# Kernel tuning notes

Measured on AMD Instinct MI355X. Metric: run time of the kernel, lower is better.

Reference implementation:

```python
import jax, jax.numpy as jnp
import numpy as np

N_VN = 8000
N_CN = 4000
DV = 3
DC = 6
BATCH = 1250
CODERATE = 0.5
NUM_ITER = 5
LLR_MAX = 20.0
EPS = 1e-12


def _build_graph():
    # regular (3,6) Tanner graph: 3 layers, each layer gives every VN one edge
    # and every CN two edges (n = 2m).
    rng = np.random.RandomState(0)
    vn = np.tile(np.arange(N_VN, dtype=np.int32), DV)
    cn_layers = []
    for _ in range(DV):
        cn_layers.append(rng.permutation(np.repeat(np.arange(N_CN, dtype=np.int32), 2)))
    cn = np.concatenate(cn_layers)
    return vn, cn


def setup_inputs() -> dict:
    key = jax.random.key(0)
    k1, = jax.random.split(key, 1)
    vn, cn = _build_graph()
    noise = jax.random.normal(k1, (BATCH, N_VN), dtype=jnp.float32)
    weights = jnp.ones((DV * N_VN,), dtype=jnp.float32)  # trainable edge weights, init 1
    return {
        "noise": noise,
        "weights": weights,
        "vn_idx": jnp.asarray(vn),
        "cn_idx": jnp.asarray(cn),
        "ebno_db": 4,
    }


def _bp_forward(noise, weights, vn_idx, cn_idx, ebno_db):
    B, n = noise.shape
    m = n // 2
    # ebnodb2no with 1 bit/symbol
    no = 1.0 / (10.0 ** (ebno_db / 10.0) * CODERATE)
    sigma2 = 4.0 / no
    # GaussianPriorSource: llr = log(p(x=1)/p(x=0)) for all-zero codeword
    llr = (-sigma2 / 2.0) + jnp.sqrt(sigma2) * noise  # [B, n]
    # decoder works internally with log(p0/p1); messages kept as [E, B]
    L = -llr.T  # [n, B]
    msg_vn = L[vn_idx]  # [E, B] initial VN->CN messages
    w = weights[:, None]

    loss = jnp.float32(0.0)
    c_hat = None
    for _ in range(NUM_ITER):
        # ---- check node update (boxplus, leave-one-out in log domain) ----
        mw = jnp.clip(msg_vn * w, -LLR_MAX, LLR_MAX)
        t = jnp.tanh(mw / 2.0)  # [E, B]
        log_t = jnp.log(jnp.maximum(jnp.abs(t), EPS))
        neg = (t < 0).astype(jnp.float32)
        sum_log = jax.ops.segment_sum(log_t, cn_idx, num_segments=m)  # [m, B]
        sum_neg = jax.ops.segment_sum(neg, cn_idx, num_segments=m)
        parity = jnp.mod(sum_neg[cn_idx] - neg, 2.0)
        sign = 1.0 - 2.0 * parity
        mag = jnp.exp(sum_log[cn_idx] - log_t)
        prod = jnp.clip(sign * mag, -1.0 + 1e-7, 1.0 - 1e-7)
        msg_cn = 2.0 * jnp.arctanh(prod)  # [E, B] CN->VN messages
        # ---- variable node update + marginalization ----
        x_tot = L + jax.ops.segment_sum(msg_cn, vn_idx, num_segments=n)  # [n, B]
        msg_vn = x_tot[vn_idx] - msg_cn
        c_hat = -x_tot.T  # back to log(p1/p0) convention, [B, n]
        # BCE(from_logits) with all-zero labels -> mean softplus(logits)
        loss = loss + jnp.mean(jax.nn.softplus(c_hat))
    loss = loss / NUM_ITER
    c = jnp.zeros((B, n), dtype=jnp.float32)
    return c, c_hat, llr, loss


def reference(noise, weights, vn_idx, cn_idx, ebno_db):
    return _bp_forward(noise, weights, vn_idx, cn_idx, ebno_db)
```

## Files before the change

kernel.cpp:

```cpp
#include <hip/hip_runtime.h>
#include <math.h>

constexpr int N_VN   = 8000;
constexpr int N_CN   = 4000;
constexpr int DV     = 3;
constexpr int DC     = 6;
constexpr int EDGES  = N_VN * DV;
constexpr int BATCH  = 1250;
constexpr int NUM_ITER = 5;
constexpr float LLR_MAX = 20.0f;
constexpr float MSGMAX = 16.635532f;
constexpr float FFLOOR = 2e-12f;

constexpr int SLOT_STRIDE = 7;
constexpr int MTPB  = 1024;
constexpr int VNPT  = (N_VN + MTPB - 1) / MTPB;

__device__ __forceinline__ float pack_ex(float mv, float w) {
    float mw = fminf(fmaxf(mv * w, -LLR_MAX), LLR_MAX);
    float ex = __expf(-fabsf(mw));
    unsigned sgn = __float_as_uint(mw) & 0x80000000u;
    return __uint_as_float(__float_as_uint(ex) | sgn);
}

__global__ __launch_bounds__(256) void build_graph_k(const int* __restrict__ cn_idx,
                                                     int* __restrict__ cnt,
                                                     int* __restrict__ epos) {
    int e = blockIdx.x * 256 + threadIdx.x;
    if (e >= EDGES) return;
    int c = cn_idx[e];
    int slot = atomicAdd(&cnt[c], 1);
    epos[e] = c * SLOT_STRIDE + slot;
}

__global__ __launch_bounds__(MTPB) void bp_mega_k(const float* __restrict__ noise,
                                                  const float* __restrict__ weights,
                                                  const int* __restrict__ epos,
                                                  const int* __restrict__ ebno,
                                                  float* __restrict__ llr_out,
                                                  float* __restrict__ chat_out,
                                                  float* __restrict__ loss_part) {
    __shared__ float eL[N_CN * SLOT_STRIDE];
    __shared__ float hs[2];
    __shared__ float red[MTPB / 64];

    const int b   = blockIdx.x;
    const int tid = threadIdx.x;

    if (tid == 0) {
        double sig2 = 2.0 * pow(10.0, (double)ebno[0] * 0.1);
        hs[0] = (float)(sig2 * 0.5);
        hs[1] = (float)sqrt(sig2);
    }
    __syncthreads();
    const float h = hs[0], s = hs[1];

    const float* nrow = noise    + (size_t)b * N_VN;
    float*       lrow = llr_out  + (size_t)b * N_VN;
    float*       crow = chat_out + (size_t)b * N_VN;

    float Lreg[VNPT];
    int   pp[VNPT][DV];
    float ww[VNPT][DV];
    #pragma unroll
    for (int r = 0; r < VNPT; ++r) {
        int v = tid + r * MTPB;
        if (v < N_VN) {
            float nv  = nrow[v];
            float llr = fmaf(s, nv, -h);
            lrow[v]   = llr;
            Lreg[r]   = -llr;
            #pragma unroll
            for (int l = 0; l < DV; ++l) {
                int e = v + l * N_VN;
                pp[r][l] = epos[e];
                ww[r][l] = weights[e];
                eL[pp[r][l]] = pack_ex(Lreg[r], ww[r][l]);
            }
        }
    }

    float lossacc = 0.0f;
    for (int it = 0; it < NUM_ITER; ++it) {
        __syncthreads();
        for (int c = tid; c < N_CN; c += MTPB) {
            float* base = eL + c * SLOT_STRIDE;
            float se[DC], f[DC], d[DC];
            float num = 1.0f, den = 1.0f;
            unsigned sx = 0u;
            #pragma unroll
            for (int j = 0; j < DC; ++j) {
                se[j] = base[j];
                float ex = fabsf(se[j]);
                f[j] = fmaxf(1.0f - ex, FFLOOR);
                d[j] = 1.0f + ex;
                num *= f[j];
                den *= d[j];
                sx  ^= __float_as_uint(se[j]);
            }
            float T = __fdividef(num, den);
            #pragma unroll
            for (int j = 0; j < DC; ++j) {
                float g  = T * d[j];
                float r  = __fdividef(f[j] + g, f[j] - g);
                float ma = fminf(__logf(r), MSGMAX);
                unsigned sg = (sx ^ __float_as_uint(se[j])) & 0x80000000u;
                base[j] = __uint_as_float(__float_as_uint(ma) ^ sg);
            }
        }
        __syncthreads();
        const bool wr = (it != NUM_ITER - 1);
        #pragma unroll
        for (int r = 0; r < VNPT; ++r) {
            int v = tid + r * MTPB;
            if (v < N_VN) {
                float m0 = eL[pp[r][0]];
                float m1 = eL[pp[r][1]];
                float m2 = eL[pp[r][2]];
                float xt = Lreg[r] + m0 + m1 + m2;
                if (wr) {
                    eL[pp[r][0]] = pack_ex(xt - m0, ww[r][0]);
                    eL[pp[r][1]] = pack_ex(xt - m1, ww[r][1]);
                    eL[pp[r][2]] = pack_ex(xt - m2, ww[r][2]);
                } else {
                    crow[v] = -xt;
                }
                lossacc += fmaxf(-xt, 0.0f) + __logf(1.0f + __expf(-fabsf(xt)));
            }
        }
    }

    #pragma unroll
    for (int off = 32; off > 0; off >>= 1)
        lossacc += __shfl_down(lossacc, off, 64);
    int lane = tid & 63, wid = tid >> 6;
    if (lane == 0) red[wid] = lossacc;
    __syncthreads();
    if (tid == 0) {
        float ssum = 0.0f;
        #pragma unroll
        for (int i = 0; i < MTPB / 64; ++i) ssum += red[i];
        loss_part[b] = ssum;
    }
}

__global__ __launch_bounds__(256) void loss_final_k(const float* __restrict__ lp,
                                                    float* __restrict__ out_loss) {
    double s = 0.0;
    for (int i = threadIdx.x; i < BATCH; i += 256) s += (double)lp[i];
    #pragma unroll
    for (int off = 32; off > 0; off >>= 1)
        s += __shfl_down(s, off, 64);
    __shared__ double red[4];
    int lane = threadIdx.x & 63, wid = threadIdx.x >> 6;
    if (lane == 0) red[wid] = s;
    __syncthreads();
    if (threadIdx.x == 0)
        out_loss[0] = (float)((red[0] + red[1] + red[2] + red[3]) /
                              ((double)NUM_ITER * (double)BATCH * (double)N_VN));
}

extern "C" void kernel_launch(void* const* d_in, const int* in_sizes, int n_in,
                              void* d_out, int out_size, void* d_ws, size_t ws_size,
                              hipStream_t stream) {
    const float* noise   = (const float*)d_in[0];
    const float* weights = (const float*)d_in[1];
    const int* cn_idx    = (const int*)d_in[3];
    const int* ebno      = (const int*)d_in[4];

    float* out      = (float*)d_out;
    float* out_c    = out;
    float* out_chat = out + 10000000;
    float* out_llr  = out + 20000000;
    float* out_loss = out + 30000000;

    char* ws = (char*)d_ws;
    int*   epos      = (int*)(ws);
    int*   cn_cnt    = (int*)(ws + 96000);
    float* loss_part = (float*)(ws + 112000);

    hipMemsetAsync(cn_cnt, 0, N_CN * sizeof(int), stream);
    build_graph_k<<<dim3((EDGES + 255) / 256), dim3(256), 0, stream>>>(cn_idx, cn_cnt, epos);

    bp_mega_k<<<dim3(BATCH), dim3(MTPB), 0, stream>>>(noise, weights, epos, ebno,
                                                      out_llr, out_chat, loss_part);

    loss_final_k<<<dim3(1), dim3(256), 0, stream>>>(loss_part, out_loss);
    hipMemsetAsync(out_c, 0, 10000000 * sizeof(float), stream);
}
```

Baseline: 400.5 us.

## Quantize edge messages to int16 in LDS and fuse zero-fill into decoder

Stores the per-edge messages in shared memory as 16-bit fixed-point values instead of floats, halving LDS use so more blocks can reside per CU (launch bounds now request 8 waves per EU). Edge positions and weights are reloaded from global memory each iteration instead of being held in registers, which lowers register pressure. The zero output tensor is now written inside the main kernel rather than by a separate memset. The change adds fixed-point quantization error on the messages and extra exp and conversion work in the check-node update.

```diff
diff --git a/kernel.cpp b/kernel.cpp
--- a/kernel.cpp
+++ b/kernel.cpp
@@ -11,16 +11,16 @@
 constexpr float LLR_MAX = 20.0f;
 constexpr float MSGMAX = 16.635532f;
 constexpr float FFLOOR = 2e-12f;
+constexpr float QSCALE = 32767.0f / 20.0f;
+constexpr float QINV   = 20.0f / 32767.0f;
 
 constexpr int SLOT_STRIDE = 7;
 constexpr int MTPB  = 1024;
 constexpr int VNPT  = (N_VN + MTPB - 1) / MTPB;
 
-__device__ __forceinline__ float pack_ex(float mv, float w) {
+__device__ __forceinline__ short quant_mw(float mv, float w) {
     float mw = fminf(fmaxf(mv * w, -LLR_MAX), LLR_MAX);
-    float ex = __expf(-fabsf(mw));
-    unsigned sgn = __float_as_uint(mw) & 0x80000000u;
-    return __uint_as_float(__float_as_uint(ex) | sgn);
+    return (short)__float2int_rn(mw * QSCALE);
 }
 
 __global__ __launch_bounds__(256) void build_graph_k(const int* __restrict__ cn_idx,
@@ -33,14 +33,15 @@
     epos[e] = c * SLOT_STRIDE + slot;
 }
 
-__global__ __launch_bounds__(MTPB) void bp_mega_k(const float* __restrict__ noise,
-                                                  const float* __restrict__ weights,
-                                                  const int* __restrict__ epos,
-                                                  const int* __restrict__ ebno,
-                                                  float* __restrict__ llr_out,
-                                                  float* __restrict__ chat_out,
-                                                  float* __restrict__ loss_part) {
-    __shared__ float eL[N_CN * SLOT_STRIDE];
+__global__ __launch_bounds__(MTPB, 8) void bp_mega_k(const float* __restrict__ noise,
+                                                     const float* __restrict__ weights,
+                                                     const int* __restrict__ epos,
+                                                     const int* __restrict__ ebno,
+                                                     float* __restrict__ llr_out,
+                                                     float* __restrict__ chat_out,
+                                                     float* __restrict__ c_out,
+                                                     float* __restrict__ loss_part) {
+    __shared__ short eS[N_CN * SLOT_STRIDE];
     __shared__ float hs[2];
     __shared__ float red[MTPB / 64];
 
@@ -58,24 +59,22 @@
     const float* nrow = noise    + (size_t)b * N_VN;
     float*       lrow = llr_out  + (size_t)b * N_VN;
     float*       crow = chat_out + (size_t)b * N_VN;
+    float*       zrow = c_out    + (size_t)b * N_VN;
 
     float Lreg[VNPT];
-    int   pp[VNPT][DV];
-    float ww[VNPT][DV];
     #pragma unroll
     for (int r = 0; r < VNPT; ++r) {
         int v = tid + r * MTPB;
-        if (v < N_VN) {
+        if (r < VNPT - 1 || v < N_VN) {
             float nv  = nrow[v];
             float llr = fmaf(s, nv, -h);
             lrow[v]   = llr;
+            zrow[v]   = 0.0f;
             Lreg[r]   = -llr;
             #pragma unroll
             for (int l = 0; l < DV; ++l) {
                 int e = v + l * N_VN;
-                pp[r][l] = epos[e];
-                ww[r][l] = weights[e];
-                eL[pp[r][l]] = pack_ex(Lreg[r], ww[r][l]);
+                eS[epos[e]] = quant_mw(Lreg[r], weights[e]);
             }
         }
     }
@@ -83,29 +82,36 @@
     float lossacc = 0.0f;
     for (int it = 0; it < NUM_ITER; ++it) {
         __syncthreads();
-        for (int c = tid; c < N_CN; c += MTPB) {
-            float* base = eL + c * SLOT_STRIDE;
-            float se[DC], f[DC], d[DC];
-            float num = 1.0f, den = 1.0f;
-            unsigned sx = 0u;
-            #pragma unroll
-            for (int j = 0; j < DC; ++j) {
-                se[j] = base[j];
-                float ex = fabsf(se[j]);
-                f[j] = fmaxf(1.0f - ex, FFLOOR);
-                d[j] = 1.0f + ex;
-                num *= f[j];
-                den *= d[j];
-                sx  ^= __float_as_uint(se[j]);
-            }
-            float T = __fdividef(num, den);
-            #pragma unroll
-            for (int j = 0; j < DC; ++j) {
-                float g  = T * d[j];
-                float r  = __fdividef(f[j] + g, f[j] - g);
-                float ma = fminf(__logf(r), MSGMAX);
-                unsigned sg = (sx ^ __float_as_uint(se[j])) & 0x80000000u;
-                base[j] = __uint_as_float(__float_as_uint(ma) ^ sg);
+        #pragma unroll
+        for (int k = 0; k < 4; ++k) {
+            int c = tid + k * MTPB;
+            if (k < 3 || c < N_CN) {
+                short* base = eS + c * SLOT_STRIDE;
+                short q[DC];
+                float f[DC];
+                float num = 1.0f, den = 1.0f;
+                unsigned sx = 0u;
+                #pragma unroll
+                for (int j = 0; j < DC; ++j) {
+                    q[j] = base[j];
+                    float mw = (float)q[j] * QINV;
+                    float ex = __expf(-fabsf(mw));
+                    float fl = fmaxf(1.0f - ex, FFLOOR);
+                    f[j] = fl;
+                    num *= fl;
+                    den *= (2.0f - fl);
+                    sx  ^= (unsigned)(int)q[j];
+                }
+                float T = __fdividef(num, den);
+                #pragma unroll
+                for (int j = 0; j < DC; ++j) {
+                    float g  = T * (2.0f - f[j]);
+                    float r2 = __fdividef(f[j] + g, f[j] - g);
+                    float ma = fminf(__logf(r2), MSGMAX);
+                    unsigned sg = (sx ^ (unsigned)(int)q[j]) & 0x80000000u;
+                    float msg = __uint_as_float(__float_as_uint(ma) ^ sg);
+                    base[j] = (short)__float2int_rn(msg * QSCALE);
+                }
             }
         }
         __syncthreads();
@@ -113,15 +119,17 @@
         #pragma unroll
         for (int r = 0; r < VNPT; ++r) {
             int v = tid + r * MTPB;
-            if (v < N_VN) {
-                float m0 = eL[pp[r][0]];
-                float m1 = eL[pp[r][1]];
-                float m2 = eL[pp[r][2]];
+            if (r < VNPT - 1 || v < N_VN) {
+                int e0 = v, e1 = v + N_VN, e2 = v + 2 * N_VN;
+                int p0 = epos[e0], p1 = epos[e1], p2 = epos[e2];
+                float m0 = (float)eS[p0] * QINV;
+                float m1 = (float)eS[p1] * QINV;
+                float m2 = (float)eS[p2] * QINV;
                 float xt = Lreg[r] + m0 + m1 + m2;
                 if (wr) {
-                    eL[pp[r][0]] = pack_ex(xt - m0, ww[r][0]);
-                    eL[pp[r][1]] = pack_ex(xt - m1, ww[r][1]);
-                    eL[pp[r][2]] = pack_ex(xt - m2, ww[r][2]);
+                    eS[p0] = quant_mw(xt - m0, weights[e0]);
+                    eS[p1] = quant_mw(xt - m1, weights[e1]);
+                    eS[p2] = quant_mw(xt - m2, weights[e2]);
                 } else {
                     crow[v] = -xt;
                 }
@@ -183,8 +191,7 @@
     build_graph_k<<<dim3((EDGES + 255) / 256), dim3(256), 0, stream>>>(cn_idx, cn_cnt, epos);
 
     bp_mega_k<<<dim3(BATCH), dim3(MTPB), 0, stream>>>(noise, weights, epos, ebno,
-                                                      out_llr, out_chat, loss_part);
+                                                      out_llr, out_chat, out_c, loss_part);
 
     loss_final_k<<<dim3(1), dim3(256), 0, stream>>>(loss_part, out_loss);
-    hipMemsetAsync(out_c, 0, 10000000 * sizeof(float), stream);
 }
```

Measured after the change: 573.3 us. +43.1%, slower.
